# Optimization experiments

Measured on AMD Instinct MI355X. Metric: run time of the kernel, lower is better.

## Reference

```python
import jax, jax.numpy as jnp
import numpy as np
import math

BIT = 8
N_HEAD = 12

def quantize_k(x, k=BIT):
    # DoReFa k-bit uniform quantizer with straight-through estimator
    n = float(2 ** k - 1)
    q = jnp.round(x * n) / n
    return x + jax.lax.stop_gradient(q - x)

def weight_quant(w, k=BIT):
    # DoReFa weight quantization: tanh normalize to [0,1], quantize, map back to [-1,1]
    t = jnp.tanh(w)
    t = t / (2.0 * jnp.max(jnp.abs(t))) + 0.5
    return 2.0 * quantize_k(t, k) - 1.0

def act_quant(x, k=BIT):
    # DoReFa activation quantization: clamp to [0,1] then k-bit quantize
    return quantize_k(jnp.clip(x, 0.0, 1.0), k)

def setup_inputs() -> dict:
    key = jax.random.key(0)
    k1, k2, k3 = jax.random.split(key, 3)
    B, S, NX = 8, 1024, 768
    x = jax.random.normal(k1, (B, S, NX), dtype=jnp.float32)
    W_attn = 0.02 * jax.random.normal(k2, (NX, 3 * NX), dtype=jnp.float32)
    b_attn = jnp.zeros((3 * NX,), dtype=jnp.float32)
    W_proj = 0.02 * jax.random.normal(k3, (NX, NX), dtype=jnp.float32)
    b_proj = jnp.zeros((NX,), dtype=jnp.float32)
    return {"x": x, "W_attn": W_attn, "b_attn": b_attn, "W_proj": W_proj, "b_proj": b_proj}

def reference(x, W_attn, b_attn, W_proj, b_proj):
    B, S, NX = x.shape
    H = N_HEAD
    hd = NX // H
    # quantized c_attn (Conv1D)
    qkv = jnp.einsum('bsn,nf->bsf', x, weight_quant(W_attn)) + b_attn  # [B,S,3*NX]
    q, k, v = jnp.split(qkv, 3, axis=-1)
    def split_heads(t):
        return t.reshape(B, S, H, hd).transpose(0, 2, 1, 3)  # [B,H,S,hd]
    q = act_quant(split_heads(q))
    k = act_quant(split_heads(k))
    v = act_quant(split_heads(v))
    # manual causal attention, scale=True
    w = jnp.einsum('bhqd,bhkd->bhqk', q, k) / math.sqrt(hd)  # [B,H,S,S]
    mask = jnp.tril(jnp.ones((S, S), dtype=x.dtype))
    w = w * mask - 10000.0 * (1.0 - mask)
    w = jax.nn.softmax(w, axis=-1)
    a = jnp.einsum('bhqk,bhkd->bhqd', w, v)  # [B,H,S,hd]
    a = a.transpose(0, 2, 1, 3).reshape(B, S, NX)  # merge heads
    a = jnp.einsum('bsn,nf->bsf', a, weight_quant(W_proj)) + b_proj
    # present = stack(key.transpose(-2,-1), value) -> both [B,H,S,hd]
    present = jnp.stack((k, v))
    return (a, present)
```

## Files before the change

kernel.cpp:

```cpp
#include <hip/hip_runtime.h>
#include <math.h>

#define B_   8
#define S_   1024
#define NXc  768
#define H_   12
#define HDc  64
#define M_   (B_*S_)
#define NQKV (3*NXc)

typedef __attribute__((ext_vector_type(8))) short short8;
typedef __attribute__((ext_vector_type(8))) _Float16 half8;
typedef __attribute__((ext_vector_type(4))) float f32x4;

__device__ inline unsigned short f2h(float f) {
  union { _Float16 h; unsigned short u; } c;
  c.h = (_Float16)f;
  return c.u;
}

__device__ inline void gl_lds16(const unsigned short* g, unsigned short* l) {
  __builtin_amdgcn_global_load_lds(
      (const __attribute__((address_space(1))) void*)g,
      (__attribute__((address_space(3))) void*)l, 16, 0, 0);
}

static const size_t UA_OFF_F  = 0;
static const size_t UA_F_CNT  = ((size_t)NQKV * NXc + 1) / 2;
static const size_t UP_OFF_F  = UA_OFF_F + UA_F_CNT;
static const size_t UP_F_CNT  = ((size_t)NXc * NXc + 1) / 2;
static const size_t QH_OFF_F  = UP_OFF_F + UP_F_CNT;
static const size_t HALF_CNT  = ((size_t)M_ * NXc + 1) / 2;
static const size_t KH_OFF_F  = QH_OFF_F + HALF_CNT;
static const size_t VHT_OFF_F = KH_OFF_F + HALF_CNT;
static const size_t AHF_OFF_F = VHT_OFF_F + HALF_CNT;
static const size_t SC_OFF    = AHF_OFF_F + HALF_CNT;
static const size_t WS_FLOATS_NEEDED = SC_OFF + 2;

__global__ void k_maxtanh2(const float* __restrict__ wa, const float* __restrict__ wp,
                           unsigned int* __restrict__ out) {
  const int which = blockIdx.y;
  const float* w = which ? wp : wa;
  const int n = which ? (NXc * NXc) : (NXc * NQKV);
  float mx = 0.f;
  for (int i = blockIdx.x * blockDim.x + threadIdx.x; i < n;
       i += gridDim.x * blockDim.x)
    mx = fmaxf(mx, fabsf(tanhf(w[i])));
#pragma unroll
  for (int off = 32; off > 0; off >>= 1)
    mx = fmaxf(mx, __shfl_xor(mx, off));
  if ((threadIdx.x & 63) == 0)
    atomicMax(out + which, __float_as_uint(mx));
}

__global__ __launch_bounds__(256) void k_quantw_t(
    const float* __restrict__ w, unsigned short* __restrict__ ut,
    int K, int N, const unsigned int* __restrict__ gmax_bits) {
  __shared__ unsigned short Ut[64][72];
  const float inv2m = 0.5f / __uint_as_float(*gmax_bits);
  const int k0 = blockIdx.y * 64, n0 = blockIdx.x * 64;
  const int t = threadIdx.x;
  const int r = t >> 4, c4 = (t & 15) * 4;
#pragma unroll
  for (int rr = 0; rr < 4; ++rr) {
    int row = rr * 16 + r;
    float4 f = *(const float4*)(w + (size_t)(k0 + row) * N + n0 + c4);
    float fv[4] = {f.x, f.y, f.z, f.w};
#pragma unroll
    for (int j = 0; j < 4; ++j) {
      float tq = tanhf(fv[j]) * inv2m + 0.5f;
      float u = 2.0f * rintf(tq * 255.0f) - 255.0f;
      Ut[c4 + j][row] = f2h(u);
    }
  }
  __syncthreads();
#pragma unroll
  for (int rep = 0; rep < 2; ++rep) {
    int c = t + rep * 256;
    int n = c >> 3, slot = c & 7;
    short8 v = *(const short8*)&Ut[n][slot * 8];
    *(short8*)(ut + (size_t)(n0 + n) * K + k0 + slot * 8) = v;
  }
}

__global__ __launch_bounds__(256) void k_xhalf(
    const float* __restrict__ x, unsigned short* __restrict__ xh, int n8) {
  int i = blockIdx.x * 256 + threadIdx.x;
  if (i >= n8) return;
  const float* src = x + (size_t)i * 8;
  float4 f0 = *(const float4*)src;
  float4 f1 = *(const float4*)(src + 4);
  float fv[8] = {f0.x, f0.y, f0.z, f0.w, f1.x, f1.y, f1.z, f1.w};
  union { short8 v; unsigned short u[8]; } o;
#pragma unroll
  for (int j = 0; j < 8; ++j) o.u[j] = f2h(fv[j]);
  *(short8*)(xh + (size_t)i * 8) = o.v;
}

__global__ __launch_bounds__(512, 4) void k_gemm_qkv(
    const unsigned short* __restrict__ xh, const unsigned short* __restrict__ ua,
    const float* __restrict__ bias,
    unsigned short* __restrict__ qh, unsigned short* __restrict__ kh,
    unsigned short* __restrict__ vht, float* __restrict__ kq, float* __restrict__ vq) {
  __shared__ __align__(16) unsigned short SMEM[3 * (4096 + 8192)];
  unsigned short* Ahb3 = SMEM;
  unsigned short* Bsb3 = SMEM + 3 * 4096;
  unsigned short* T    = SMEM;

  const int bid = blockIdx.x;
  const int swz = (bid & 7) * 72 + (bid >> 3);
  const int bm = swz / 9, bn = swz % 9;
  const int part = bn / 3;

  const int t = threadIdx.x;
  const int w = t >> 6, lane = t & 63;
  const int wm = w >> 2, wn = w & 3;
  const int g = lane >> 4, ln = lane & 15;

  const unsigned short* Ab = xh + (size_t)bm * 128 * NXc;
  const unsigned short* Bb = ua + (size_t)bn * 256 * NXc;

  const int srow = t >> 2;
  const int aco  = (((t & 3) ^ ((t >> 3) & 3)) << 3);
  const int rsw  = ((g ^ ((ln >> 1) & 3)) << 3);

  f32x4 acc[4][4];
#pragma unroll
  for (int i = 0; i < 4; ++i)
#pragma unroll
    for (int j = 0; j < 4; ++j) acc[i][j] = (f32x4)(0.f);

  auto STAGE = [&](int tk, int buf) {
    const int k0 = tk * 32;
    unsigned short* Ah = Ahb3 + buf * 4096;
    unsigned short* Bs = Bsb3 + buf * 8192;
    gl_lds16(Ab + (size_t)srow * NXc + k0 + aco, &Ah[t * 8]);
    gl_lds16(Bb + (size_t)srow * NXc + k0 + aco, &Bs[t * 8]);
    gl_lds16(Bb + (size_t)(srow + 128) * NXc + k0 + aco, &Bs[(512 + t) * 8]);
  };
  auto COMPUTE = [&](int buf) {
    const unsigned short* Ah = Ahb3 + buf * 4096;
    const unsigned short* Bs = Bsb3 + buf * 8192;
    half8 bfrag[4];
#pragma unroll
    for (int nf = 0; nf < 4; ++nf)
      bfrag[nf] = *(const half8*)&Bs[(wn * 64 + nf * 16 + ln) * 32 + rsw];
#pragma unroll
    for (int mf = 0; mf < 4; ++mf) {
      half8 ah = *(const half8*)&Ah[(wm * 64 + mf * 16 + ln) * 32 + rsw];
#pragma unroll
      for (int nf = 0; nf < 4; ++nf)
        acc[mf][nf] = __builtin_amdgcn_mfma_f32_16x16x32_f16(ah, bfrag[nf], acc[mf][nf], 0, 0, 0);
    }
  };

  STAGE(0, 0);
  STAGE(1, 1);
  for (int tk = 0; tk < 22; ++tk) {
    asm volatile("s_waitcnt vmcnt(3)" ::: "memory");
    __builtin_amdgcn_s_barrier();
    __builtin_amdgcn_sched_barrier(0);
    STAGE(tk + 2, (tk + 2) % 3);
    COMPUTE(tk % 3);
  }
  asm volatile("s_waitcnt vmcnt(3)" ::: "memory");
  __builtin_amdgcn_s_barrier();
  __builtin_amdgcn_sched_barrier(0);
  COMPUTE(22 % 3);
  asm volatile("s_waitcnt vmcnt(0)" ::: "memory");
  __builtin_amdgcn_s_barrier();
  __builtin_amdgcn_sched_barrier(0);
  COMPUTE(23 % 3);

  const float inv255 = 1.0f / 255.0f;
  if (part == 2) {
    __syncthreads();
#pragma unroll
    for (int mf = 0; mf < 4; ++mf) {
      int row0 = bm * 128 + wm * 64 + mf * 16 + g * 4;
#pragma unroll
      for (int nf = 0; nf < 4; ++nf) {
        int c = wn * 64 + nf * 16 + ln;
        int col = bn * 256 + c;
        float bv255 = bias[col] * 255.0f;
        int ff = col - 2 * NXc;
        int h = ff >> 6, d = ff & 63;
#pragma unroll
        for (int r = 0; r < 4; ++r) {
          float y255 = rintf(fminf(fmaxf(acc[mf][nf][r] + bv255, 0.f), 255.f));
          int row = row0 + r;
          int b = row >> 10, s = row & 1023;
          vq[(((size_t)b * H_ + h) * S_ + s) * HDc + d] = y255 * inv255;
          int sl = wm * 64 + mf * 16 + g * 4 + r;
          T[c * 136 + sl] = f2h(y255);
        }
      }
    }
    __syncthreads();
    const int bB = bm >> 3;
    const int s0 = (bm & 7) * 128;
    const int h0 = (bn - 6) * 4;
#pragma unroll
    for (int rep = 0; rep < 8; ++rep) {
      int idx = rep * 512 + t;
      int c = idx >> 4, sc = idx & 15;
      short8 v = *(const short8*)&T[c * 136 + sc * 8];
      int h = h0 + (c >> 6), d = c & 63;
      *(short8*)(vht + (((size_t)bB * H_ + h) * HDc + d) * S_ + s0 + sc * 8) = v;
    }
  } else {
    __syncthreads();
#pragma unroll
    for (int mf = 0; mf < 4; ++mf) {
      int lrow0 = wm * 64 + mf * 16 + g * 4;
#pragma unroll
      for (int nf = 0; nf < 4; ++nf) {
        int lcol = wn * 64 + nf * 16 + ln;
        float bv255 = bias[bn * 256 + lcol] * 255.0f;
#pragma unroll
        for (int r = 0; r < 4; ++r) {
          float y255 = rintf(fminf(fmaxf(acc[mf][nf][r] + bv255, 0.f), 255.f));
          T[(lrow0 + r) * 264 + lcol] = f2h(y255);
        }
      }
    }
    __syncthreads();
#pragma unroll
    for (int rep = 0; rep < 8; ++rep) {
      int idx = rep * 512 + t;
      int row = idx >> 5, cc = idx & 31;
      short8 v = *(const short8*)&T[row * 264 + cc * 8];
      int grow = bm * 128 + row;
      int b = grow >> 10, s = grow & 1023;
      int col = bn * 256 + cc * 8;
      int ff = col - part * NXc;
      int h = ff >> 6, d0 = ff & 63;
      size_t dst = (((size_t)b * H_ + h) * S_ + s) * HDc + d0;
      if (part == 0) {
        *(short8*)(qh + dst) = v;
      } else {
        *(short8*)(kh + dst) = v;
        union { short8 s8; half8 h8; } cvt; cvt.s8 = v;
        float4 f0, f1;
        f0.x = (float)cvt.h8[0] * inv255; f0.y = (float)cvt.h8[1] * inv255;
        f0.z = (float)cvt.h8[2] * inv255; f0.w = (float)cvt.h8[3] * inv255;
        f1.x = (float)cvt.h8[4] * inv255; f1.y = (float)cvt.h8[5] * inv255;
        f1.z = (float)cvt.h8[6] * inv255; f1.w = (float)cvt.h8[7] * inv255;
        *(float4*)(kq + dst) = f0;
        *(float4*)(kq + dst + 4) = f1;
      }
    }
  }
}

__global__ __launch_bounds__(256, 4) void k_gemm_proj(
    const unsigned short* __restrict__ ahf, const unsigned short* __restrict__ up,
    const float* __restrict__ bias, float* __restrict__ Cout) {
  __shared__ __align__(16) unsigned short SMEM[3 * (2048 + 4096)];
  unsigned short* Ahb3 = SMEM;
  unsigned short* Bsb3 = SMEM + 3 * 2048;

  const int bid = blockIdx.x;
  const int swz = (bid & 7) * 96 + (bid >> 3);
  const int bm = swz / 6, bn = swz % 6;

  const int t = threadIdx.x;
  const int w = t >> 6, lane = t & 63;
  const int wm = w >> 1, wn = w & 1;
  const int g = lane >> 4, ln = lane & 15;

  const unsigned short* Ab = ahf + (size_t)bm * 64 * NXc;
  const unsigned short* Bb = up + (size_t)bn * 128 * NXc;

  const int srow = t >> 2;
  const int aco  = (((t & 3) ^ ((t >> 3) & 3)) << 3);
  const int rsw  = ((g ^ ((ln >> 1) & 3)) << 3);

  f32x4 acc[2][4];
#pragma unroll
  for (int i = 0; i < 2; ++i)
#pragma unroll
    for (int j = 0; j < 4; ++j) acc[i][j] = (f32x4)(0.f);

  auto STAGE = [&](int tk, int buf) {
    const int k0 = tk * 32;
    unsigned short* Ah = Ahb3 + buf * 2048;
    unsigned short* Bs = Bsb3 + buf * 4096;
    gl_lds16(Ab + (size_t)srow * NXc + k0 + aco, &Ah[t * 8]);
    gl_lds16(Bb + (size_t)srow * NXc + k0 + aco, &Bs[t * 8]);
    gl_lds16(Bb + (size_t)(srow + 64) * NXc + k0 + aco, &Bs[(256 + t) * 8]);
  };
  auto COMPUTE = [&](int buf) {
    const unsigned short* Ah = Ahb3 + buf * 2048;
    const unsigned short* Bs = Bsb3 + buf * 4096;
    half8 bfrag[4];
#pragma unroll
    for (int nf = 0; nf < 4; ++nf)
      bfrag[nf] = *(const half8*)&Bs[(wn * 64 + nf * 16 + ln) * 32 + rsw];
#pragma unroll
    for (int mf = 0; mf < 2; ++mf) {
      half8 ah = *(const half8*)&Ah[(wm * 32 + mf * 16 + ln) * 32 + rsw];
#pragma unroll
      for (int nf = 0; nf < 4; ++nf)
        acc[mf][nf] = __builtin_amdgcn_mfma_f32_16x16x32_f16(ah, bfrag[nf], acc[mf][nf], 0, 0, 0);
    }
  };

  STAGE(0, 0);
  STAGE(1, 1);
  for (int tk = 0; tk < 22; ++tk) {
    asm volatile("s_waitcnt vmcnt(3)" ::: "memory");
    __builtin_amdgcn_s_barrier();
    __builtin_amdgcn_sched_barrier(0);
    STAGE(tk + 2, (tk + 2) % 3);
    COMPUTE(tk % 3);
  }
  asm volatile("s_waitcnt vmcnt(3)" ::: "memory");
  __builtin_amdgcn_s_barrier();
  __builtin_amdgcn_sched_barrier(0);
  COMPUTE(22 % 3);
  asm volatile("s_waitcnt vmcnt(0)" ::: "memory");
  __builtin_amdgcn_s_barrier();
  __builtin_amdgcn_sched_barrier(0);
  COMPUTE(23 % 3);

  const float inv255 = 1.0f / 255.0f;
#pragma unroll
  for (int mf = 0; mf < 2; ++mf) {
    int row0 = bm * 64 + wm * 32 + mf * 16 + g * 4;
#pragma unroll
    for (int nf = 0; nf < 4; ++nf) {
      int col = bn * 128 + wn * 64 + nf * 16 + ln;
      float bv = bias[col];
#pragma unroll
      for (int r = 0; r < 4; ++r)
        Cout[(size_t)(row0 + r) * NXc + col] = acc[mf][nf][r] * inv255 + bv;
    }
  }
}

__global__ __launch_bounds__(256) void k_attn_pair(
    const unsigned short* __restrict__ qh, const unsigned short* __restrict__ kh,
    const unsigned short* __restrict__ vht, unsigned short* __restrict__ ahf) {
  __shared__ __align__(16) unsigned short Ks[2][64 * 64];
  __shared__ __align__(16) unsigned short Vt[2][64 * 64];
  __shared__ __align__(16) unsigned short Pp[4 * 16 * 64];

  const int bid = blockIdx.x;
  const int gidx = (bid & 7) * 96 + (bid >> 3);
  const int hid = gidx >> 3;
  const int p = gidx & 7;
  const int b = hid / H_, h = hid - b * H_;

  const size_t hoff = (size_t)hid * S_ * HDc;
  const unsigned short* qhp = qh + hoff;
  const unsigned short* khp = kh + hoff;
  const unsigned short* vhp = vht + hoff;

  const int t = threadIdx.x;
  const int w = t >> 6, lane = t & 63;
  const int g = lane >> 4, ln = lane & 15;

  const int r0 = t >> 3, c0 = (((t & 7) ^ (r0 & 7)) << 3);
  const int r1 = 32 + (t >> 3), c1 = (((t & 7) ^ (r1 & 7)) << 3);

  auto STAGE = [&](int jb, int buf) {
    gl_lds16(khp + (size_t)(jb * 64 + r0) * HDc + c0, &Ks[buf][t * 8]);
    gl_lds16(khp + (size_t)(jb * 64 + r1) * HDc + c1, &Ks[buf][(256 + t) * 8]);
    gl_lds16(vhp + (size_t)r0 * S_ + jb * 64 + c0, &Vt[buf][t * 8]);
    gl_lds16(vhp + (size_t)r1 * S_ + jb * 64 + c1, &Vt[buf][(256 + t) * 8]);
  };

  const float SCALE = 1.0f / (255.0f * 255.0f * 8.0f);

  int iq = p;
  half8 qfrag[2];
  {
    const unsigned short* qr = qhp + (size_t)(iq * 64 + w * 16 + ln) * HDc;
    qfrag[0] = *(const half8*)(qr + g * 8);
    qfrag[1] = *(const half8*)(qr + 32 + g * 8);
  }

  float l[4];
  f32x4 accO[4];
#pragma unroll
  for (int r = 0; r < 4; ++r) l[r] = 0.f;
#pragma unroll
  for (int nf = 0; nf < 4; ++nf) accO[nf] = (f32x4)(0.f);

  auto WRITEOUT = [&]() {
#pragma unroll
    for (int off = 1; off < 16; off <<= 1)
#pragma unroll
      for (int r = 0; r < 4; ++r) l[r] += __shfl_xor(l[r], off);
#pragma unroll
    for (int r = 0; r < 4; ++r) {
      float inv = 1.0f / (255.0f * l[r]);
      size_t row = (size_t)b * S_ + iq * 64 + w * 16 + g * 4 + r;
#pragma unroll
      for (int nf = 0; nf < 4; ++nf)
        ahf[row * NXc + h * HDc + nf * 16 + ln] = f2h(accO[nf][r] * inv);
    }
  };

  STAGE(0, 0);
  int jb = 0;
  for (int i = 0; i < 17; ++i) {
    const int buf = i & 1;
    __syncthreads();
    if (i + 1 < 17) {
      int njb = (i + 1 <= p) ? (i + 1) : (i - p);
      STAGE(njb, buf ^ 1);
    }

    f32x4 accS[4];
#pragma unroll
    for (int nf = 0; nf < 4; ++nf) accS[nf] = (f32x4)(0.f);
#pragma unroll
    for (int ks = 0; ks < 2; ++ks)
#pragma unroll
      for (int nf = 0; nf < 4; ++nf) {
        int kvr = nf * 16 + ln;
        half8 bk = *(const half8*)&Ks[buf][kvr * 64 + ((ks * 32 + g * 8) ^ ((kvr & 7) << 3))];
        accS[nf] = __builtin_amdgcn_mfma_f32_16x16x32_f16(qfrag[ks], bk, accS[nf], 0, 0, 0);
      }

    float pr[4][4];
    if (jb == iq) {
      const int grow = iq * 64 + w * 16 + g * 4;
      const int gcol = jb * 64 + ln;
#pragma unroll
      for (int nf = 0; nf < 4; ++nf)
#pragma unroll
        for (int r = 0; r < 4; ++r) {
          float pv = (gcol + nf * 16 > grow + r) ? 0.f : __expf(accS[nf][r] * SCALE);
          pr[nf][r] = pv;
          l[r] += pv;
        }
    } else {
#pragma unroll
      for (int nf = 0; nf < 4; ++nf)
#pragma unroll
        for (int r = 0; r < 4; ++r) {
          float pv = __expf(accS[nf][r] * SCALE);
          pr[nf][r] = pv;
          l[r] += pv;
        }
    }

#pragma unroll
    for (int nf = 0; nf < 4; ++nf)
#pragma unroll
      for (int r = 0; r < 4; ++r) {
        int prow = g * 4 + r;
        Pp[w * 1024 + prow * 64 + ((nf * 16 + ln) ^ ((prow & 7) << 3))] = f2h(pr[nf][r]);
      }

#pragma unroll
    for (int ks = 0; ks < 2; ++ks) {
      half8 pa = *(const half8*)&Pp[w * 1024 + ln * 64 + ((ks * 32 + g * 8) ^ ((ln & 7) << 3))];
#pragma unroll
      for (int nf = 0; nf < 4; ++nf) {
        int d = nf * 16 + ln;
        half8 bv = *(const half8*)&Vt[buf][d * 64 + ((ks * 32 + g * 8) ^ ((d & 7) << 3))];
        accO[nf] = __builtin_amdgcn_mfma_f32_16x16x32_f16(pa, bv, accO[nf], 0, 0, 0);
      }
    }

    if (i == p) {
      WRITEOUT();
#pragma unroll
      for (int r = 0; r < 4; ++r) l[r] = 0.f;
#pragma unroll
      for (int nf = 0; nf < 4; ++nf) accO[nf] = (f32x4)(0.f);
      iq = 15 - p;
      const unsigned short* qr2 = qhp + (size_t)(iq * 64 + w * 16 + ln) * HDc;
      qfrag[0] = *(const half8*)(qr2 + g * 8);
      qfrag[1] = *(const half8*)(qr2 + 32 + g * 8);
    } else if (i == 16) {
      WRITEOUT();
    }
    jb = (i + 1 <= p) ? (i + 1) : (i - p);
  }
}

extern "C" void kernel_launch(void* const* d_in, const int* in_sizes, int n_in,
                              void* d_out, int out_size, void* d_ws, size_t ws_size,
                              hipStream_t stream) {
  const float* x      = (const float*)d_in[0];
  const float* W_attn = (const float*)d_in[1];
  const float* b_attn = (const float*)d_in[2];
  const float* W_proj = (const float*)d_in[3];
  const float* b_proj = (const float*)d_in[4];

  float* out = (float*)d_out;
  float* ws  = (float*)d_ws;
  if (ws_size < WS_FLOATS_NEEDED * sizeof(float)) return;

  float* a_out = out;
  float* k_out = out + (size_t)M_ * NXc;
  float* v_out = k_out + (size_t)M_ * NXc;

  unsigned short* ua  = (unsigned short*)(ws + UA_OFF_F);
  unsigned short* up  = (unsigned short*)(ws + UP_OFF_F);
  unsigned short* qh  = (unsigned short*)(ws + QH_OFF_F);
  unsigned short* kh  = (unsigned short*)(ws + KH_OFF_F);
  unsigned short* vht = (unsigned short*)(ws + VHT_OFF_F);
  unsigned short* ahf = (unsigned short*)(ws + AHF_OFF_F);
  unsigned int* sc = (unsigned int*)(ws + SC_OFF);

  unsigned short* xh = ahf;

  hipMemsetAsync(sc, 0, 2 * sizeof(unsigned int), stream);

  k_maxtanh2<<<dim3(128, 2), 256, 0, stream>>>(W_attn, W_proj, sc);

  k_quantw_t<<<dim3(NQKV / 64, NXc / 64), 256, 0, stream>>>(W_attn, ua, NXc, NQKV, sc);
  k_quantw_t<<<dim3(NXc / 64, NXc / 64), 256, 0, stream>>>(W_proj, up, NXc, NXc, sc + 1);

  k_xhalf<<<(M_ * NXc / 8 + 255) / 256, 256, 0, stream>>>(x, xh, M_ * NXc / 8);

  k_gemm_qkv<<<(NQKV / 256) * (M_ / 128), 512, 0, stream>>>(
      xh, ua, b_attn, qh, kh, vht, k_out, v_out);

  k_attn_pair<<<768, 256, 0, stream>>>(qh, kh, vht, ahf);

  k_gemm_proj<<<(NXc / 128) * (M_ / 64), 256, 0, stream>>>(ahf, up, b_proj, a_out);
}
```

Baseline: 143.8 us.

## Merge prep kernels and give QKV GEMM waves a wider 64x128 tile

Fuses the tanh-max reduction with the x-to-half conversion into one launch, and merges the two weight-quantize launches into one kernel, cutting the launch count from five to three. The QKV GEMM drops from 512 to 256 threads per block, so each wave computes a 64x128 sub-tile with 32 accumulators and issues twice as many async loads per stage. The sched_barrier calls are removed. This raises register pressure and halves the number of waves available to hide latency in the GEMM.

```diff
diff --git a/kernel.cpp b/kernel.cpp
--- a/kernel.cpp
+++ b/kernel.cpp
@@ -37,28 +37,53 @@
 static const size_t SC_OFF    = AHF_OFF_F + HALF_CNT;
 static const size_t WS_FLOATS_NEEDED = SC_OFF + 2;
 
-__global__ void k_maxtanh2(const float* __restrict__ wa, const float* __restrict__ wp,
-                           unsigned int* __restrict__ out) {
-  const int which = blockIdx.y;
-  const float* w = which ? wp : wa;
-  const int n = which ? (NXc * NXc) : (NXc * NQKV);
-  float mx = 0.f;
-  for (int i = blockIdx.x * blockDim.x + threadIdx.x; i < n;
-       i += gridDim.x * blockDim.x)
-    mx = fmaxf(mx, fabsf(tanhf(w[i])));
-#pragma unroll
-  for (int off = 32; off > 0; off >>= 1)
-    mx = fmaxf(mx, __shfl_xor(mx, off));
-  if ((threadIdx.x & 63) == 0)
-    atomicMax(out + which, __float_as_uint(mx));
-}
-
-__global__ __launch_bounds__(256) void k_quantw_t(
-    const float* __restrict__ w, unsigned short* __restrict__ ut,
-    int K, int N, const unsigned int* __restrict__ gmax_bits) {
+__global__ __launch_bounds__(256) void k_prep(
+    const float* __restrict__ x, unsigned short* __restrict__ xh,
+    const float* __restrict__ wa, const float* __restrict__ wp,
+    unsigned int* __restrict__ out) {
+  const int bid = blockIdx.x;
+  if (bid < 3072) {
+    int i = bid * 256 + threadIdx.x;
+    const float* src = x + (size_t)i * 8;
+    float4 f0 = *(const float4*)src;
+    float4 f1 = *(const float4*)(src + 4);
+    float fv[8] = {f0.x, f0.y, f0.z, f0.w, f1.x, f1.y, f1.z, f1.w};
+    union { short8 v; unsigned short u[8]; } o;
+#pragma unroll
+    for (int j = 0; j < 8; ++j) o.u[j] = f2h(fv[j]);
+    *(short8*)(xh + (size_t)i * 8) = o.v;
+  } else {
+    const int which = (bid - 3072) >> 7;
+    const int xb = (bid - 3072) & 127;
+    const float* w = which ? wp : wa;
+    const int n = which ? (NXc * NXc) : (NXc * NQKV);
+    float mx = 0.f;
+    for (int i = xb * 256 + threadIdx.x; i < n; i += 128 * 256)
+      mx = fmaxf(mx, fabsf(tanhf(w[i])));
+#pragma unroll
+    for (int off = 32; off > 0; off >>= 1)
+      mx = fmaxf(mx, __shfl_xor(mx, off));
+    if ((threadIdx.x & 63) == 0)
+      atomicMax(out + which, __float_as_uint(mx));
+  }
+}
+
+__global__ __launch_bounds__(256) void k_quantw2(
+    const float* __restrict__ wa, const float* __restrict__ wp,
+    unsigned short* __restrict__ ua, unsigned short* __restrict__ up,
+    const unsigned int* __restrict__ sc) {
   __shared__ unsigned short Ut[64][72];
-  const float inv2m = 0.5f / __uint_as_float(*gmax_bits);
-  const int k0 = blockIdx.y * 64, n0 = blockIdx.x * 64;
+  const int bid = blockIdx.x;
+  const int isp = (bid >= 432);
+  const float* w = isp ? wp : wa;
+  unsigned short* ut = isp ? up : ua;
+  const int N = isp ? NXc : NQKV;
+  const int K = NXc;
+  const int idx = isp ? (bid - 432) : bid;
+  const int nb = isp ? 12 : 36;
+  const int bx = idx % nb, by = idx / nb;
+  const float inv2m = 0.5f / __uint_as_float(sc[isp]);
+  const int k0 = by * 64, n0 = bx * 64;
   const int t = threadIdx.x;
   const int r = t >> 4, c4 = (t & 15) * 4;
 #pragma unroll
@@ -83,26 +108,12 @@
   }
 }
 
-__global__ __launch_bounds__(256) void k_xhalf(
-    const float* __restrict__ x, unsigned short* __restrict__ xh, int n8) {
-  int i = blockIdx.x * 256 + threadIdx.x;
-  if (i >= n8) return;
-  const float* src = x + (size_t)i * 8;
-  float4 f0 = *(const float4*)src;
-  float4 f1 = *(const float4*)(src + 4);
-  float fv[8] = {f0.x, f0.y, f0.z, f0.w, f1.x, f1.y, f1.z, f1.w};
-  union { short8 v; unsigned short u[8]; } o;
-#pragma unroll
-  for (int j = 0; j < 8; ++j) o.u[j] = f2h(fv[j]);
-  *(short8*)(xh + (size_t)i * 8) = o.v;
-}
-
-__global__ __launch_bounds__(512, 4) void k_gemm_qkv(
+__global__ __launch_bounds__(256, 2) void k_gemm_qkv(
     const unsigned short* __restrict__ xh, const unsigned short* __restrict__ ua,
     const float* __restrict__ bias,
     unsigned short* __restrict__ qh, unsigned short* __restrict__ kh,
     unsigned short* __restrict__ vht, float* __restrict__ kq, float* __restrict__ vq) {
-  __shared__ __align__(16) unsigned short SMEM[3 * (4096 + 8192)];
+  __shared__ __align__(16) unsigned short SMEM[3 * 12288];
   unsigned short* Ahb3 = SMEM;
   unsigned short* Bsb3 = SMEM + 3 * 4096;
   unsigned short* T    = SMEM;
@@ -114,7 +125,7 @@
 
   const int t = threadIdx.x;
   const int w = t >> 6, lane = t & 63;
-  const int wm = w >> 2, wn = w & 3;
+  const int wm = w >> 1, wn = w & 1;
   const int g = lane >> 4, ln = lane & 15;
 
   const unsigned short* Ab = xh + (size_t)bm * 128 * NXc;
@@ -124,32 +135,34 @@
   const int aco  = (((t & 3) ^ ((t >> 3) & 3)) << 3);
   const int rsw  = ((g ^ ((ln >> 1) & 3)) << 3);
 
-  f32x4 acc[4][4];
+  f32x4 acc[4][8];
 #pragma unroll
   for (int i = 0; i < 4; ++i)
 #pragma unroll
-    for (int j = 0; j < 4; ++j) acc[i][j] = (f32x4)(0.f);
+    for (int j = 0; j < 8; ++j) acc[i][j] = (f32x4)(0.f);
 
   auto STAGE = [&](int tk, int buf) {
     const int k0 = tk * 32;
     unsigned short* Ah = Ahb3 + buf * 4096;
     unsigned short* Bs = Bsb3 + buf * 8192;
     gl_lds16(Ab + (size_t)srow * NXc + k0 + aco, &Ah[t * 8]);
-    gl_lds16(Bb + (size_t)srow * NXc + k0 + aco, &Bs[t * 8]);
-    gl_lds16(Bb + (size_t)(srow + 128) * NXc + k0 + aco, &Bs[(512 + t) * 8]);
+    gl_lds16(Ab + (size_t)(srow + 64) * NXc + k0 + aco, &Ah[(256 + t) * 8]);
+#pragma unroll
+    for (int rr = 0; rr < 4; ++rr)
+      gl_lds16(Bb + (size_t)(srow + rr * 64) * NXc + k0 + aco, &Bs[(rr * 256 + t) * 8]);
   };
   auto COMPUTE = [&](int buf) {
     const unsigned short* Ah = Ahb3 + buf * 4096;
     const unsigned short* Bs = Bsb3 + buf * 8192;
-    half8 bfrag[4];
-#pragma unroll
-    for (int nf = 0; nf < 4; ++nf)
-      bfrag[nf] = *(const half8*)&Bs[(wn * 64 + nf * 16 + ln) * 32 + rsw];
+    half8 bfrag[8];
+#pragma unroll
+    for (int nf = 0; nf < 8; ++nf)
+      bfrag[nf] = *(const half8*)&Bs[(wn * 128 + nf * 16 + ln) * 32 + rsw];
 #pragma unroll
     for (int mf = 0; mf < 4; ++mf) {
       half8 ah = *(const half8*)&Ah[(wm * 64 + mf * 16 + ln) * 32 + rsw];
 #pragma unroll
-      for (int nf = 0; nf < 4; ++nf)
+      for (int nf = 0; nf < 8; ++nf)
         acc[mf][nf] = __builtin_amdgcn_mfma_f32_16x16x32_f16(ah, bfrag[nf], acc[mf][nf], 0, 0, 0);
     }
   };
@@ -157,19 +170,16 @@
   STAGE(0, 0);
   STAGE(1, 1);
   for (int tk = 0; tk < 22; ++tk) {
-    asm volatile("s_waitcnt vmcnt(3)" ::: "memory");
+    asm volatile("s_waitcnt vmcnt(6)" ::: "memory");
     __builtin_amdgcn_s_barrier();
-    __builtin_amdgcn_sched_barrier(0);
     STAGE(tk + 2, (tk + 2) % 3);
     COMPUTE(tk % 3);
   }
-  asm volatile("s_waitcnt vmcnt(3)" ::: "memory");
+  asm volatile("s_waitcnt vmcnt(6)" ::: "memory");
   __builtin_amdgcn_s_barrier();
-  __builtin_amdgcn_sched_barrier(0);
   COMPUTE(22 % 3);
   asm volatile("s_waitcnt vmcnt(0)" ::: "memory");
   __builtin_amdgcn_s_barrier();
-  __builtin_amdgcn_sched_barrier(0);
   COMPUTE(23 % 3);
 
   const float inv255 = 1.0f / 255.0f;
@@ -179,8 +189,8 @@
     for (int mf = 0; mf < 4; ++mf) {
       int row0 = bm * 128 + wm * 64 + mf * 16 + g * 4;
 #pragma unroll
-      for (int nf = 0; nf < 4; ++nf) {
-        int c = wn * 64 + nf * 16 + ln;
+      for (int nf = 0; nf < 8; ++nf) {
+        int c = wn * 128 + nf * 16 + ln;
         int col = bn * 256 + c;
         float bv255 = bias[col] * 255.0f;
         int ff = col - 2 * NXc;
@@ -201,12 +211,12 @@
     const int s0 = (bm & 7) * 128;
     const int h0 = (bn - 6) * 4;
 #pragma unroll
-    for (int rep = 0; rep < 8; ++rep) {
-      int idx = rep * 512 + t;
-      int c = idx >> 4, sc = idx & 15;
-      short8 v = *(const short8*)&T[c * 136 + sc * 8];
+    for (int rep = 0; rep < 16; ++rep) {
+      int idx = rep * 256 + t;
+      int c = idx >> 4, sc2 = idx & 15;
+      short8 v = *(const short8*)&T[c * 136 + sc2 * 8];
       int h = h0 + (c >> 6), d = c & 63;
-      *(short8*)(vht + (((size_t)bB * H_ + h) * HDc + d) * S_ + s0 + sc * 8) = v;
+      *(short8*)(vht + (((size_t)bB * H_ + h) * HDc + d) * S_ + s0 + sc2 * 8) = v;
     }
   } else {
     __syncthreads();
@@ -214,8 +224,8 @@
     for (int mf = 0; mf < 4; ++mf) {
       int lrow0 = wm * 64 + mf * 16 + g * 4;
 #pragma unroll
-      for (int nf = 0; nf < 4; ++nf) {
-        int lcol = wn * 64 + nf * 16 + ln;
+      for (int nf = 0; nf < 8; ++nf) {
+        int lcol = wn * 128 + nf * 16 + ln;
         float bv255 = bias[bn * 256 + lcol] * 255.0f;
 #pragma unroll
         for (int r = 0; r < 4; ++r) {
@@ -226,8 +236,8 @@
     }
     __syncthreads();
 #pragma unroll
-    for (int rep = 0; rep < 8; ++rep) {
-      int idx = rep * 512 + t;
+    for (int rep = 0; rep < 16; ++rep) {
+      int idx = rep * 256 + t;
       int row = idx >> 5, cc = idx & 31;
       short8 v = *(const short8*)&T[row * 264 + cc * 8];
       int grow = bm * 128 + row;
@@ -513,14 +523,11 @@
 
   hipMemsetAsync(sc, 0, 2 * sizeof(unsigned int), stream);
 
-  k_maxtanh2<<<dim3(128, 2), 256, 0, stream>>>(W_attn, W_proj, sc);
-
-  k_quantw_t<<<dim3(NQKV / 64, NXc / 64), 256, 0, stream>>>(W_attn, ua, NXc, NQKV, sc);
-  k_quantw_t<<<dim3(NXc / 64, NXc / 64), 256, 0, stream>>>(W_proj, up, NXc, NXc, sc + 1);
-
-  k_xhalf<<<(M_ * NXc / 8 + 255) / 256, 256, 0, stream>>>(x, xh, M_ * NXc / 8);
-
-  k_gemm_qkv<<<(NQKV / 256) * (M_ / 128), 512, 0, stream>>>(
+  k_prep<<<3328, 256, 0, stream>>>(x, xh, W_attn, W_proj, sc);
+
+  k_quantw2<<<576, 256, 0, stream>>>(W_attn, W_proj, ua, up, sc);
+
+  k_gemm_qkv<<<(NQKV / 256) * (M_ / 128), 256, 0, stream>>>(
       xh, ua, b_attn, qh, kh, vht, k_out, v_out);
 
   k_attn_pair<<<768, 256, 0, stream>>>(qh, kh, vht, ahf);
```

Result: faster. 137.6 us (-4.3%).
